# Kernel optimization log

Measured on AMD Instinct MI355X. Metric: run time of the kernel, lower is better.

## Reference

```python
import jax, jax.numpy as jnp
import numpy as np

BN_EPS = 1e-5

def _bn(h, gamma, beta):
    # training-mode BatchNorm1d over node dim, biased variance (as torch)
    m = jnp.mean(h, axis=0)
    v = jnp.var(h, axis=0)
    return (h - m) * jax.lax.rsqrt(v + BN_EPS) * gamma + beta

def _gin(x, edge_index, W, b, n_nodes):
    # PyG GINConv (eps=0): h = Linear(x + sum_{j in N(i)} x_j)
    src, dst = edge_index[0], edge_index[1]
    agg = jax.ops.segment_sum(x[src], dst, num_segments=n_nodes)
    return (x + agg) @ W + b

def setup_inputs() -> dict:
    key = jax.random.key(0)
    ks = jax.random.split(key, 16)
    N, E, D, H, G = 50000, 800000, 128, 256, 64
    x = jax.random.normal(ks[0], (N, D), dtype=jnp.float32)
    edge_index = jax.random.randint(ks[1], (2, E), 0, N, dtype=jnp.int64)
    batch = jnp.sort(jax.random.randint(ks[2], (N,), 0, G, dtype=jnp.int64))
    s = 0.05
    return {
        "x": x, "edge_index": edge_index, "batch": batch, "num_graphs": G,
        "W1": jax.random.normal(ks[3], (D, H), jnp.float32) * s,
        "b1": jnp.zeros((H,), jnp.float32),
        "W2": jax.random.normal(ks[4], (H, H), jnp.float32) * s,
        "b2": jnp.zeros((H,), jnp.float32),
        "W3": jax.random.normal(ks[5], (H, H), jnp.float32) * s,
        "b3": jnp.zeros((H,), jnp.float32),
        "g1": jnp.ones((H,), jnp.float32), "be1": jnp.zeros((H,), jnp.float32),
        "g2": jnp.ones((H,), jnp.float32), "be2": jnp.zeros((H,), jnp.float32),
        "g3": jnp.ones((H,), jnp.float32), "be3": jnp.zeros((H,), jnp.float32),
        "fcW1": jax.random.normal(ks[6], (H, H), jnp.float32) * s,
        "fcb1": jnp.zeros((H,), jnp.float32),
        "fcW2": jax.random.normal(ks[7], (H, 1), jnp.float32) * s,
        "fcb2": jnp.zeros((1,), jnp.float32),
    }

def reference(x, edge_index, batch, num_graphs, W1, b1, W2, b2, W3, b3,
              g1, be1, g2, be2, g3, be3, fcW1, fcb1, fcW2, fcb2):
    n_nodes = x.shape[0]
    # dropout treated as identity (eval / deterministic)
    x1 = jax.nn.relu(_bn(_gin(x, edge_index, W1, b1, n_nodes), g1, be1))
    x2 = jax.nn.relu(_bn(_gin(x1, edge_index, W2, b2, n_nodes), g2, be2)) + x1
    x3 = jax.nn.relu(_bn(_gin(x2, edge_index, W3, b3, n_nodes), g3, be3)) + x2
    # global mean pool over graphs
    sums = jax.ops.segment_sum(x3, batch, num_segments=num_graphs)
    cnt = jax.ops.segment_sum(jnp.ones((n_nodes,), x3.dtype), batch, num_segments=num_graphs)
    pooled = sums / jnp.maximum(cnt, 1.0)[:, None]
    h = jax.nn.relu(pooled @ fcW1 + fcb1)
    return h @ fcW2 + fcb2
```

## Files before the change

### kernel.cpp

```cpp
#include <hip/hip_runtime.h>
#include <hip/hip_bf16.h>
#include <stdint.h>

#define HDIM 256
#define NGRAPH 64
#define NSH 16

typedef short s16x8 __attribute__((ext_vector_type(8)));
typedef float f32x4 __attribute__((ext_vector_type(4)));
typedef unsigned int u32x4 __attribute__((ext_vector_type(4)));

union U8 { u32x4 v; unsigned short s[8]; };

__device__ __forceinline__ float bf2f(unsigned short u){
    union { unsigned int i; float f; } x; x.i = ((unsigned int)u) << 16; return x.f;
}
__device__ __forceinline__ unsigned short f2bf(float f){
    union { float f; unsigned int i; } x; x.f = f;
    unsigned int r = x.i + 0x7fffu + ((x.i >> 16) & 1u);
    return (unsigned short)(r >> 16);
}
__device__ __forceinline__ float ldf(const void* p, int i, int f32){
    return f32 ? ((const float*)p)[i] : bf2f(((const unsigned short*)p)[i]);
}

__global__ void zero_detect_kernel(int* __restrict__ p, int n,
                                   const unsigned short* __restrict__ x,
                                   const int* __restrict__ ei, const int* __restrict__ batch,
                                   int E, int N, int* __restrict__ flags){
    int i = blockIdx.x * 256 + threadIdx.x;
    if (i < n) p[i] = 0;
    if (i == 0){
        int c = 0;
        for (int k = 0; k < 128; k++){
            unsigned e = (x[2 * k] >> 7) & 0xFFu;
            if (e >= 100u && e <= 140u) c++;
        }
        flags[0] = (c < 96) ? 1 : 0;
        int z = (ei[2*E - 1] == 0) && (ei[2*E - 3] == 0) && (ei[2*E - 5] == 0) && (ei[2*E - 7] == 0);
        flags[1] = z ? 1 : 0;
        flags[2] = (batch[N - 1] == 0) ? 1 : 0;
    }
}

__global__ void hist_kernel(const int* __restrict__ ei, int E, int N,
                            const int* __restrict__ flags, int* __restrict__ deg){
    int is64 = flags[1];
    int base = blockIdx.x * 1024;
    #pragma unroll
    for (int k = 0; k < 4; k++){
        int e = base + k * 256 + threadIdx.x;
        if (e < E){
            int d = is64 ? ei[2 * E + 2 * e] : ei[E + e];
            if ((unsigned)d < (unsigned)N) atomicAdd(&deg[d], 1);
        }
    }
}

__global__ void scan1_kernel(const int* __restrict__ deg, int N,
                             int* __restrict__ incl, int* __restrict__ bsums){
    __shared__ int sm[256];
    int t = threadIdx.x;
    int i = blockIdx.x * 256 + t;
    int v = (i < N) ? deg[i] : 0;
    sm[t] = v; __syncthreads();
    for (int off = 1; off < 256; off <<= 1){
        int tv = (t >= off) ? sm[t - off] : 0;
        __syncthreads();
        sm[t] += tv;
        __syncthreads();
    }
    if (i < N) incl[i] = sm[t];
    if (t == 255) bsums[blockIdx.x] = sm[255];
}

__global__ void scan23_kernel(const int* __restrict__ deg, int N, int E, int nb,
                              const int* __restrict__ bsums, int* __restrict__ rowptr){
    __shared__ int sm[256];
    int t = threadIdx.x;
    int bid = blockIdx.x;
    sm[t] = (t < nb && t < bid) ? bsums[t] : 0;
    __syncthreads();
    for (int s = 128; s > 0; s >>= 1){
        if (t < s) sm[t] += sm[t + s];
        __syncthreads();
    }
    int prefix = sm[0];
    int i = bid * 256 + t;
    if (i < N) rowptr[i] = rowptr[i] - deg[i] + prefix;
    if (i == 0) rowptr[N] = E;
}

__global__ void fill_kernel(const int* __restrict__ ei, int E, int N,
                            const int* __restrict__ flags,
                            const int* __restrict__ rowptr, int* __restrict__ fillc,
                            int* __restrict__ csr){
    int is64 = flags[1];
    int base = blockIdx.x * 1024;
    #pragma unroll
    for (int k = 0; k < 4; k++){
        int e = base + k * 256 + threadIdx.x;
        if (e < E){
            int d = is64 ? ei[2 * E + 2 * e] : ei[E + e];
            int s = is64 ? ei[2 * e]         : ei[e];
            if ((unsigned)d < (unsigned)N){
                int p = atomicAdd(&fillc[d], 1);
                csr[rowptr[d] + p] = s;
            }
        }
    }
}

__global__ void prep_kernel(const void* __restrict__ W1, unsigned short* __restrict__ Wp1,
                            const void* __restrict__ W2, unsigned short* __restrict__ Wp2,
                            const void* __restrict__ W3, unsigned short* __restrict__ Wp3,
                            const void* __restrict__ x, unsigned short* __restrict__ Xc,
                            int nx8, const int* __restrict__ flags){
    int bid = blockIdx.x;
    int f32 = flags[0];
    if (bid < 640){
        const void* W; unsigned short* Wp; int base;
        if (bid < 128)      { W = W1; Wp = Wp1; base = bid; }
        else if (bid < 384) { W = W2; Wp = Wp2; base = bid - 128; }
        else                { W = W3; Wp = Wp3; base = bid - 384; }
        int idx = base * 256 + threadIdx.x;
        int k2 = idx & 31;
        int nn = (idx >> 5) & 255;
        int kc = idx >> 13;
        Wp[idx] = f2bf(ldf(W, (kc * 32 + k2) * 256 + nn, f32));
    } else {
        int i = (bid - 640) * 256 + threadIdx.x;
        if (i >= nx8) return;
        int base = i * 8;
        unsigned short o[8];
        if (f32){
            const float* s = (const float*)x + base;
            float4 a = *(const float4*)s;
            float4 b = *(const float4*)(s + 4);
            o[0]=f2bf(a.x); o[1]=f2bf(a.y); o[2]=f2bf(a.z); o[3]=f2bf(a.w);
            o[4]=f2bf(b.x); o[5]=f2bf(b.y); o[6]=f2bf(b.z); o[7]=f2bf(b.w);
        } else {
            *(uint4*)o = *(const uint4*)((const unsigned short*)x + base);
        }
        *(uint4*)&Xc[base] = *(uint4*)o;
    }
}

template<int C>
__global__ __launch_bounds__(256) void agg_vec(const unsigned short* __restrict__ feat, int ldi,
                                               const int* __restrict__ rowptr, const int* __restrict__ csr,
                                               unsigned short* __restrict__ Y, int ldo,
                                               int n0, int n1){
    constexpr int L   = C / 8;
    constexpr int NPB = 256 / L;
    int node = n0 + blockIdx.x * NPB + threadIdx.x / L;
    int lane = threadIdx.x & (L - 1);
    if (node >= n1) return;
    int c0 = lane * 8;
    const unsigned short* base = feat + c0;

    U8 t0; t0.v = *(const u32x4*)&feat[(size_t)node * ldi + c0];
    float acc[8];
    #pragma unroll
    for (int j = 0; j < 8; j++) acc[j] = bf2f(t0.s[j]);

    int lo = rowptr[node], hi = rowptr[node + 1];
    int e = lo;
    for (; e + 3 < hi; e += 4){
        int s0 = csr[e], s1 = csr[e + 1], s2 = csr[e + 2], s3 = csr[e + 3];
        U8 ta, tb, tc, td;
        ta.v = *(const u32x4*)&base[(size_t)s0 * ldi];
        tb.v = *(const u32x4*)&base[(size_t)s1 * ldi];
        tc.v = *(const u32x4*)&base[(size_t)s2 * ldi];
        td.v = *(const u32x4*)&base[(size_t)s3 * ldi];
        #pragma unroll
        for (int j = 0; j < 8; j++)
            acc[j] += (bf2f(ta.s[j]) + bf2f(tb.s[j])) + (bf2f(tc.s[j]) + bf2f(td.s[j]));
    }
    for (; e < hi; e++){
        int s0 = csr[e];
        U8 ta; ta.v = *(const u32x4*)&base[(size_t)s0 * ldi];
        #pragma unroll
        for (int j = 0; j < 8; j++) acc[j] += bf2f(ta.s[j]);
    }
    U8 o;
    #pragma unroll
    for (int j = 0; j < 8; j++) o.s[j] = f2bf(acc[j]);
    *(u32x4*)&Y[(size_t)node * ldo + c0] = o.v;
}

#define CSTR 264
__global__ __launch_bounds__(256) void gemm_tile(
    unsigned short* __restrict__ AC, int K,
    const unsigned short* __restrict__ Bp, const void* __restrict__ bias,
    int M, const int* __restrict__ flags,
    float* __restrict__ S, float* __restrict__ Q)
{
    __shared__ __align__(16) unsigned short smem[64 * CSTR];
    __shared__ float sS[256], sQ[256];
    unsigned short* As = smem;
    unsigned short* Bs = smem + 2560;
    const int tid  = threadIdx.x;
    const int wave = tid >> 6, lane = tid & 63;
    const int quad = lane >> 4, l16 = lane & 15;
    const int m0   = blockIdx.x * 64;
    const int wn   = wave * 64;
    const bool full = (m0 + 64 <= M);
    const int f32  = flags[0];

    const f32x4 zero4 = {0.f, 0.f, 0.f, 0.f};
    f32x4 acc[4][4];
    #pragma unroll
    for (int i = 0; i < 4; i++)
        #pragma unroll
        for (int j = 0; j < 4; j++) acc[i][j] = zero4;

    const int nchunk = K >> 5;
    for (int kc8 = 0; kc8 < nchunk; kc8++){
        int kc = kc8 * 32;
        {
            int r = tid >> 2, cc = (tid & 3) * 8;
            int gr = m0 + r;
            uint4 va; va.x = va.y = va.z = va.w = 0u;
            if (full || gr < M) va = *(const uint4*)&AC[(size_t)gr * HDIM + kc + cc];
            *(uint4*)&As[r * 40 + cc] = va;
        }
        {
            const unsigned short* bc = Bp + (size_t)kc8 * 8192;
            #pragma unroll
            for (int j = 0; j < 4; j++){
                int c = tid + j * 256;
                int n = c >> 2, seg = (c & 3) * 8;
                *(uint4*)&Bs[n * 40 + seg] = *(const uint4*)&bc[c * 8];
            }
        }
        __syncthreads();
        s16x8 af[4], bfr[4];
        #pragma unroll
        for (int mt = 0; mt < 4; mt++)
            af[mt] = *(const s16x8*)&As[(mt * 16 + l16) * 40 + quad * 8];
        #pragma unroll
        for (int nt = 0; nt < 4; nt++)
            bfr[nt] = *(const s16x8*)&Bs[(wn + nt * 16 + l16) * 40 + quad * 8];
        #pragma unroll
        for (int mt = 0; mt < 4; mt++)
            #pragma unroll
            for (int nt = 0; nt < 4; nt++)
                acc[mt][nt] = __builtin_amdgcn_mfma_f32_16x16x32_bf16(af[mt], bfr[nt], acc[mt][nt], 0, 0, 0);
        __syncthreads();
    }
    #pragma unroll
    for (int nt = 0; nt < 4; nt++){
        int gc = wn + nt * 16 + l16;
        float bv = ldf(bias, gc, f32);
        float ps = 0.f, pq = 0.f;
        #pragma unroll
        for (int mt = 0; mt < 4; mt++){
            #pragma unroll
            for (int r = 0; r < 4; r++){
                int lr = mt * 16 + quad * 4 + r;
                float val = acc[mt][nt][r] + bv;
                smem[lr * CSTR + gc] = f2bf(val);
                if (full || (m0 + lr) < M){ ps += val; pq += val * val; }
            }
        }
        ps += __shfl_xor(ps, 16); ps += __shfl_xor(ps, 32);
        pq += __shfl_xor(pq, 16); pq += __shfl_xor(pq, 32);
        if (quad == 0){ sS[gc] = ps; sQ[gc] = pq; }
    }
    __syncthreads();
    #pragma unroll
    for (int j = 0; j < 8; j++){
        int lin = j * 256 + tid;
        int row = lin >> 5, coll = (lin & 31) * 8;
        int gr = m0 + row;
        if (full || gr < M)
            *(uint4*)&AC[(size_t)gr * HDIM + coll] = *(const uint4*)&smem[row * CSTR + coll];
    }
    int sid = (blockIdx.x & (NSH - 1)) * 256 + tid;
    atomicAdd(&S[sid], sS[tid]);
    atomicAdd(&Q[sid], sQ[tid]);
}

__global__ void bnrelu_kernel(const unsigned short* __restrict__ Hin,
                              const float* __restrict__ S, const float* __restrict__ Q,
                              const void* __restrict__ g, const void* __restrict__ be,
                              float invM, const int* __restrict__ flags,
                              const unsigned short* __restrict__ res,
                              unsigned short* __restrict__ Out, int total16){
    __shared__ float sscale[256], sshift[256];
    int tid = threadIdx.x;
    {
        int f32 = flags[0];
        float s = 0.f, q = 0.f;
        #pragma unroll
        for (int k = 0; k < NSH; k++){ s += S[k * 256 + tid]; q += Q[k * 256 + tid]; }
        float m  = s * invM;
        float v  = q * invM - m * m;
        float sc = ldf(g, tid, f32) * rsqrtf(v + 1e-5f);
        sscale[tid] = sc;
        sshift[tid] = ldf(be, tid, f32) - m * sc;
    }
    __syncthreads();
    int idx = blockIdx.x * 256 + tid;
    if (idx >= total16) return;
    #pragma unroll
    for (int h = 0; h < 2; h++){
        int base = idx * 16 + h * 8;
        int c = base & (HDIM - 1);
        unsigned short hv[8], rv[8], ov[8];
        *(uint4*)hv = *(const uint4*)&Hin[base];
        if (res) *(uint4*)rv = *(const uint4*)&res[base];
        #pragma unroll
        for (int j = 0; j < 8; j++){
            float v = bf2f(hv[j]) * sscale[c + j] + sshift[c + j];
            v = (v < 0.f) ? 0.f : v;
            if (res) v += bf2f(rv[j]);
            ov[j] = f2bf(v);
        }
        *(uint4*)&Out[base] = *(uint4*)ov;
    }
}

__global__ __launch_bounds__(256) void bnrelu_pool_kernel(
    const unsigned short* __restrict__ H, const unsigned short* __restrict__ res,
    const float* __restrict__ S, const float* __restrict__ Q,
    const void* __restrict__ g, const void* __restrict__ be,
    float invM, const int* __restrict__ flags,
    const int* __restrict__ batch, int N, float* __restrict__ sums)
{
    __shared__ float lsc[256], lsh[256];
    __shared__ float red[8 * 256];
    int tid = threadIdx.x;
    {
        int f32 = flags[0];
        float s = 0.f, q = 0.f;
        #pragma unroll
        for (int k = 0; k < NSH; k++){ s += S[k * 256 + tid]; q += Q[k * 256 + tid]; }
        float m  = s * invM;
        float v  = q * invM - m * m;
        float sc = ldf(g, tid, f32) * rsqrtf(v + 1e-5f);
        lsc[tid] = sc;
        lsh[tid] = ldf(be, tid, f32) - m * sc;
    }
    __syncthreads();
    int r0 = blockIdx.x * 64;
    if (r0 >= N) return;
    int r1 = min(r0 + 64, N);
    int stride = flags[2] ? 2 : 1;
    int gfirst = batch[r0 * stride];
    int glast  = batch[(r1 - 1) * stride];
    int w  = tid >> 5;
    int c0 = (tid & 31) * 8;
    float sc[8], sh[8];
    #pragma unroll
    for (int j = 0; j < 8; j++){ sc[j] = lsc[c0 + j]; sh[j] = lsh[c0 + j]; }

    float acc[8];
    #pragma unroll
    for (int j = 0; j < 8; j++) acc[j] = 0.f;

    if (gfirst == glast){
        for (int r = r0 + w; r < r1; r += 8){
            U8 hv, rv;
            hv.v = *(const u32x4*)&H[(size_t)r * HDIM + c0];
            rv.v = *(const u32x4*)&res[(size_t)r * HDIM + c0];
            #pragma unroll
            for (int j = 0; j < 8; j++){
                float v = bf2f(hv.s[j]) * sc[j] + sh[j];
                v = (v < 0.f) ? 0.f : v;
                acc[j] += v + bf2f(rv.s[j]);
            }
        }
        *(float4*)&red[w * 256 + c0]     = make_float4(acc[0], acc[1], acc[2], acc[3]);
        *(float4*)&red[w * 256 + c0 + 4] = make_float4(acc[4], acc[5], acc[6], acc[7]);
        __syncthreads();
        float tot = 0.f;
        #pragma unroll
        for (int k = 0; k < 8; k++) tot += red[k * 256 + tid];
        atomicAdd(&sums[gfirst * HDIM + tid], tot);
    } else {
        int curg = batch[min(r0 + w, r1 - 1) * stride];
        for (int r = r0 + w; r < r1; r += 8){
            int gg = batch[r * stride];
            if (gg != curg){
                #pragma unroll
                for (int j = 0; j < 8; j++){
                    if (acc[j] != 0.f) atomicAdd(&sums[curg * HDIM + c0 + j], acc[j]);
                    acc[j] = 0.f;
                }
                curg = gg;
            }
            U8 hv, rv;
            hv.v = *(const u32x4*)&H[(size_t)r * HDIM + c0];
            rv.v = *(const u32x4*)&res[(size_t)r * HDIM + c0];
            #pragma unroll
            for (int j = 0; j < 8; j++){
                float v = bf2f(hv.s[j]) * sc[j] + sh[j];
                v = (v < 0.f) ? 0.f : v;
                acc[j] += v + bf2f(rv.s[j]);
            }
        }
        #pragma unroll
        for (int j = 0; j < 8; j++)
            if (acc[j] != 0.f) atomicAdd(&sums[curg * HDIM + c0 + j], acc[j]);
    }
}

__global__ __launch_bounds__(256) void head_kernel(const float* __restrict__ sums,
                                                   const int* __restrict__ batch, int N,
                                                   const void* __restrict__ fcW1,
                                                   const void* __restrict__ fcb1,
                                                   const void* __restrict__ fcW2,
                                                   const void* __restrict__ fcb2,
                                                   void* __restrict__ out,
                                                   const int* __restrict__ flags){
    __shared__ float sp[256];
    __shared__ float red[256];
    __shared__ int scnt;
    int g = blockIdx.x, j = threadIdx.x;
    int f32 = flags[0];
    int stride = flags[2] ? 2 : 1;
    if (j == 0){
        int lo = 0, hi = N;
        while (lo < hi){ int mid = (lo + hi) >> 1; if (batch[mid * stride] < g) lo = mid + 1; else hi = mid; }
        int a = lo;
        lo = 0; hi = N;
        while (lo < hi){ int mid = (lo + hi) >> 1; if (batch[mid * stride] < g + 1) lo = mid + 1; else hi = mid; }
        scnt = lo - a;
    }
    __syncthreads();
    sp[j] = sums[g * HDIM + j] / (float)max(scnt, 1);
    __syncthreads();
    float acc = ldf(fcb1, j, f32);
    for (int k = 0; k < HDIM; k++) acc += sp[k] * ldf(fcW1, k * HDIM + j, f32);
    acc = (acc < 0.f) ? 0.f : acc;
    red[j] = acc * ldf(fcW2, j, f32);
    __syncthreads();
    for (int s = 128; s > 0; s >>= 1){
        if (j < s) red[j] += red[j + s];
        __syncthreads();
    }
    if (j == 0){
        float r = red[0] + ldf(fcb2, 0, f32);
        if (f32) ((float*)out)[g] = r;
        else     ((unsigned short*)out)[g] = f2bf(r);
    }
}

extern "C" void kernel_launch(void* const* d_in, const int* in_sizes, int n_in,
                              void* d_out, int out_size, void* d_ws, size_t ws_size,
                              hipStream_t stream)
{
    const unsigned short* x    = (const unsigned short*)d_in[0];
    const int*            ei   = (const int*)d_in[1];
    const int*            batch= (const int*)d_in[2];
    const void* W1   = d_in[4];
    const void* b1   = d_in[5];
    const void* W2   = d_in[6];
    const void* b2   = d_in[7];
    const void* W3   = d_in[8];
    const void* b3   = d_in[9];
    const void* g1   = d_in[10];
    const void* be1  = d_in[11];
    const void* g2   = d_in[12];
    const void* be2  = d_in[13];
    const void* g3   = d_in[14];
    const void* be3  = d_in[15];
    const void* fcW1 = d_in[16];
    const void* fcb1 = d_in[17];
    const void* fcW2 = d_in[18];
    const void* fcb2 = d_in[19];

    const int N = in_sizes[0] / 128;
    const int E = in_sizes[1] / 2;
    const int D = 128;

    char* p = (char*)d_ws;
    int*   deg     = (int*)p;   p += (size_t)N * 4;
    int*   fillc   = (int*)p;   p += (size_t)N * 4;
    float* stats   = (float*)p; p += 6 * NSH * 256 * 4;
    float* poolsum = (float*)p; p += NGRAPH * HDIM * 4;
    size_t zbytes  = (size_t)(p - (char*)d_ws);
    int*   flags   = (int*)p;   p += 16 * 4;
    int*   bsums   = (int*)p;   p += 256 * 4;
    int*   rowptr  = (int*)p;   p += ((size_t)N + 4) * 4;
    int*   csr     = (int*)p;   p += (size_t)E * 4;
    unsigned short* Wp1 = (unsigned short*)p; p += 256 * 128 * 2;
    unsigned short* Wp2 = (unsigned short*)p; p += 256 * 256 * 2;
    unsigned short* Wp3 = (unsigned short*)p; p += 256 * 256 * 2;
    unsigned short* B1  = (unsigned short*)p; p += (size_t)N * HDIM * 2;
    unsigned short* B2  = (unsigned short*)p; p += (size_t)N * HDIM * 2;
    unsigned short* Xc  = B1;

    float* S0 = stats + 0 * NSH * 256; float* Q0 = stats + 1 * NSH * 256;
    float* S1 = stats + 2 * NSH * 256; float* Q1 = stats + 3 * NSH * 256;
    float* S2 = stats + 4 * NSH * 256; float* Q2 = stats + 5 * NSH * 256;

    const int nbN = (N + 255) / 256;
    const int nbE4 = (E + 1023) / 1024;
    const int gM64  = (N + 63) / 64;
    const float invM = 1.0f / (float)N;
    const int total16 = N * HDIM / 16;
    const int zn = (int)(zbytes / 4);
    const int nx8 = N * D / 8;
    const int half = N / 2;

    zero_detect_kernel<<<(zn + 255) / 256, 256, 0, stream>>>((int*)d_ws, zn, x, ei, batch, E, N, flags);

    hist_kernel<<<nbE4, 256, 0, stream>>>(ei, E, N, flags, deg);
    scan1_kernel<<<nbN, 256, 0, stream>>>(deg, N, rowptr, bsums);
    scan23_kernel<<<nbN, 256, 0, stream>>>(deg, N, E, nbN, bsums, rowptr);
    fill_kernel<<<nbE4, 256, 0, stream>>>(ei, E, N, flags, rowptr, fillc, csr);

    prep_kernel<<<640 + (nx8 + 255) / 256, 256, 0, stream>>>(W1, Wp1, W2, Wp2, W3, Wp3, x, Xc, nx8, flags);

    agg_vec<128><<<(half + 15) / 16, 256, 0, stream>>>(Xc, D, rowptr, csr, B2, HDIM, 0, half);
    agg_vec<128><<<(N - half + 15) / 16, 256, 0, stream>>>(Xc, D, rowptr, csr, B2, HDIM, half, N);
    gemm_tile<<<gM64, 256, 0, stream>>>(B2, 128, Wp1, b1, N, flags, S0, Q0);
    bnrelu_kernel<<<(total16 + 255) / 256, 256, 0, stream>>>(
        B2, S0, Q0, g1, be1, invM, flags, (const unsigned short*)nullptr, B1, total16);

    agg_vec<256><<<(half + 7) / 8, 256, 0, stream>>>(B1, HDIM, rowptr, csr, B2, HDIM, 0, half);
    agg_vec<256><<<(N - half + 7) / 8, 256, 0, stream>>>(B1, HDIM, rowptr, csr, B2, HDIM, half, N);
    gemm_tile<<<gM64, 256, 0, stream>>>(B2, 256, Wp2, b2, N, flags, S1, Q1);
    bnrelu_kernel<<<(total16 + 255) / 256, 256, 0, stream>>>(
        B2, S1, Q1, g2, be2, invM, flags, B1, B1, total16);

    agg_vec<256><<<(half + 7) / 8, 256, 0, stream>>>(B1, HDIM, rowptr, csr, B2, HDIM, 0, half);
    agg_vec<256><<<(N - half + 7) / 8, 256, 0, stream>>>(B1, HDIM, rowptr, csr, B2, HDIM, half, N);
    gemm_tile<<<gM64, 256, 0, stream>>>(B2, 256, Wp3, b3, N, flags, S2, Q2);
    bnrelu_pool_kernel<<<gM64, 256, 0, stream>>>(
        B2, B1, S2, Q2, g3, be3, invM, flags, batch, N, poolsum);

    head_kernel<<<NGRAPH, 256, 0, stream>>>(poolsum, batch, N, fcW1, fcb1, fcW2, fcb2, d_out, flags);

    (void)n_in; (void)out_size; (void)ws_size;
}
```

Baseline: 526.2 us.

## Enlarge GEMM tile to 128 rows with 2x2 wave layout; merge split aggregation launches

The GEMM block now computes a 128x256 tile using a 2x2 wave grid, each wave covering 64x128. This doubles B-operand reuse per block and halves the number of blocks. The epilogue is written back in two 64-row passes through shared memory, with per-column stats accumulated by shared atomics. The aggregation kernel is also launched once over all nodes instead of as two half-range launches. Risks are higher register pressure from the 32 accumulators and lower occupancy, plus fewer blocks (~391) across the CUs.

```diff
diff --git a/kernel.cpp b/kernel.cpp
--- a/kernel.cpp
+++ b/kernel.cpp
@@ -5,6 +5,7 @@
 #define HDIM 256
 #define NGRAPH 64
 #define NSH 16
+#define CSTR 264
 
 typedef short s16x8 __attribute__((ext_vector_type(8)));
 typedef float f32x4 __attribute__((ext_vector_type(4)));
@@ -149,13 +150,12 @@
 template<int C>
 __global__ __launch_bounds__(256) void agg_vec(const unsigned short* __restrict__ feat, int ldi,
                                                const int* __restrict__ rowptr, const int* __restrict__ csr,
-                                               unsigned short* __restrict__ Y, int ldo,
-                                               int n0, int n1){
+                                               unsigned short* __restrict__ Y, int ldo, int N){
     constexpr int L   = C / 8;
     constexpr int NPB = 256 / L;
-    int node = n0 + blockIdx.x * NPB + threadIdx.x / L;
+    int node = blockIdx.x * NPB + threadIdx.x / L;
     int lane = threadIdx.x & (L - 1);
-    if (node >= n1) return;
+    if (node >= N) return;
     int c0 = lane * 8;
     const unsigned short* base = feat + c0;
 
@@ -189,7 +189,6 @@
     *(u32x4*)&Y[(size_t)node * ldo + c0] = o.v;
 }
 
-#define CSTR 264
 __global__ __launch_bounds__(256) void gemm_tile(
     unsigned short* __restrict__ AC, int K,
     const unsigned short* __restrict__ Bp, const void* __restrict__ bias,
@@ -199,27 +198,32 @@
     __shared__ __align__(16) unsigned short smem[64 * CSTR];
     __shared__ float sS[256], sQ[256];
     unsigned short* As = smem;
-    unsigned short* Bs = smem + 2560;
+    unsigned short* Bs = smem + 5120;
     const int tid  = threadIdx.x;
     const int wave = tid >> 6, lane = tid & 63;
     const int quad = lane >> 4, l16 = lane & 15;
-    const int m0   = blockIdx.x * 64;
-    const int wn   = wave * 64;
-    const bool full = (m0 + 64 <= M);
+    const int m0   = blockIdx.x * 128;
+    const int wm   = (wave & 1) * 64;
+    const int wn   = (wave >> 1) * 128;
+    const bool full = (m0 + 128 <= M);
     const int f32  = flags[0];
 
+    sS[tid] = 0.f; sQ[tid] = 0.f;
+
     const f32x4 zero4 = {0.f, 0.f, 0.f, 0.f};
-    f32x4 acc[4][4];
+    f32x4 acc[4][8];
     #pragma unroll
     for (int i = 0; i < 4; i++)
         #pragma unroll
-        for (int j = 0; j < 4; j++) acc[i][j] = zero4;
+        for (int j = 0; j < 8; j++) acc[i][j] = zero4;
 
     const int nchunk = K >> 5;
     for (int kc8 = 0; kc8 < nchunk; kc8++){
         int kc = kc8 * 32;
-        {
-            int r = tid >> 2, cc = (tid & 3) * 8;
+        #pragma unroll
+        for (int j = 0; j < 2; j++){
+            int c = tid + j * 256;
+            int r = c >> 2, cc = (c & 3) * 8;
             int gr = m0 + r;
             uint4 va; va.x = va.y = va.z = va.w = 0u;
             if (full || gr < M) va = *(const uint4*)&AC[(size_t)gr * HDIM + kc + cc];
@@ -235,47 +239,53 @@
             }
         }
         __syncthreads();
-        s16x8 af[4], bfr[4];
+        s16x8 af[4];
         #pragma unroll
         for (int mt = 0; mt < 4; mt++)
-            af[mt] = *(const s16x8*)&As[(mt * 16 + l16) * 40 + quad * 8];
-        #pragma unroll
-        for (int nt = 0; nt < 4; nt++)
-            bfr[nt] = *(const s16x8*)&Bs[(wn + nt * 16 + l16) * 40 + quad * 8];
-        #pragma unroll
-        for (int mt = 0; mt < 4; mt++)
+            af[mt] = *(const s16x8*)&As[(wm + mt * 16 + l16) * 40 + quad * 8];
+        #pragma unroll
+        for (int nt = 0; nt < 8; nt++){
+            s16x8 b = *(const s16x8*)&Bs[(wn + nt * 16 + l16) * 40 + quad * 8];
             #pragma unroll
-            for (int nt = 0; nt < 4; nt++)
-                acc[mt][nt] = __builtin_amdgcn_mfma_f32_16x16x32_bf16(af[mt], bfr[nt], acc[mt][nt], 0, 0, 0);
-        __syncthreads();
-    }
-    #pragma unroll
-    for (int nt = 0; nt < 4; nt++){
-        int gc = wn + nt * 16 + l16;
-        float bv = ldf(bias, gc, f32);
-        float ps = 0.f, pq = 0.f;
-        #pragma unroll
-        for (int mt = 0; mt < 4; mt++){
+            for (int mt = 0; mt < 4; mt++)
+                acc[mt][nt] = __builtin_amdgcn_mfma_f32_16x16x32_bf16(af[mt], b, acc[mt][nt], 0, 0, 0);
+        }
+        __syncthreads();
+    }
+    #pragma unroll
+    for (int pass = 0; pass < 2; pass++){
+        if ((wave & 1) == pass){
             #pragma unroll
-            for (int r = 0; r < 4; r++){
-                int lr = mt * 16 + quad * 4 + r;
-                float val = acc[mt][nt][r] + bv;
-                smem[lr * CSTR + gc] = f2bf(val);
-                if (full || (m0 + lr) < M){ ps += val; pq += val * val; }
+            for (int nt = 0; nt < 8; nt++){
+                int gc = wn + nt * 16 + l16;
+                float bv = ldf(bias, gc, f32);
+                float ps = 0.f, pq = 0.f;
+                #pragma unroll
+                for (int mt = 0; mt < 4; mt++){
+                    #pragma unroll
+                    for (int r = 0; r < 4; r++){
+                        int lr = mt * 16 + quad * 4 + r;
+                        int gr = m0 + pass * 64 + lr;
+                        float val = acc[mt][nt][r] + bv;
+                        smem[lr * CSTR + gc] = f2bf(val);
+                        if (full || gr < M){ ps += val; pq += val * val; }
+                    }
+                }
+                ps += __shfl_xor(ps, 16); ps += __shfl_xor(ps, 32);
+                pq += __shfl_xor(pq, 16); pq += __shfl_xor(pq, 32);
+                if (quad == 0){ atomicAdd(&sS[gc], ps); atomicAdd(&sQ[gc], pq); }
             }
         }
-        ps += __shfl_xor(ps, 16); ps += __shfl_xor(ps, 32);
-        pq += __shfl_xor(pq, 16); pq += __shfl_xor(pq, 32);
-        if (quad == 0){ sS[gc] = ps; sQ[gc] = pq; }
-    }
-    __syncthreads();
-    #pragma unroll
-    for (int j = 0; j < 8; j++){
-        int lin = j * 256 + tid;
-        int row = lin >> 5, coll = (lin & 31) * 8;
-        int gr = m0 + row;
-        if (full || gr < M)
-            *(uint4*)&AC[(size_t)gr * HDIM + coll] = *(const uint4*)&smem[row * CSTR + coll];
+        __syncthreads();
+        #pragma unroll
+        for (int j = 0; j < 8; j++){
+            int lin = j * 256 + tid;
+            int row = lin >> 5, coll = (lin & 31) * 8;
+            int gr = m0 + pass * 64 + row;
+            if (full || gr < M)
+                *(uint4*)&AC[(size_t)gr * HDIM + coll] = *(const uint4*)&smem[row * CSTR + coll];
+        }
+        __syncthreads();
     }
     int sid = (blockIdx.x & (NSH - 1)) * 256 + tid;
     atomicAdd(&S[sid], sS[tid]);
@@ -499,12 +509,12 @@
 
     const int nbN = (N + 255) / 256;
     const int nbE4 = (E + 1023) / 1024;
+    const int gM128 = (N + 127) / 128;
     const int gM64  = (N + 63) / 64;
     const float invM = 1.0f / (float)N;
     const int total16 = N * HDIM / 16;
     const int zn = (int)(zbytes / 4);
     const int nx8 = N * D / 8;
-    const int half = N / 2;
 
     zero_detect_kernel<<<(zn + 255) / 256, 256, 0, stream>>>((int*)d_ws, zn, x, ei, batch, E, N, flags);
 
@@ -515,21 +525,18 @@
 
     prep_kernel<<<640 + (nx8 + 255) / 256, 256, 0, stream>>>(W1, Wp1, W2, Wp2, W3, Wp3, x, Xc, nx8, flags);
 
-    agg_vec<128><<<(half + 15) / 16, 256, 0, stream>>>(Xc, D, rowptr, csr, B2, HDIM, 0, half);
-    agg_vec<128><<<(N - half + 15) / 16, 256, 0, stream>>>(Xc, D, rowptr, csr, B2, HDIM, half, N);
-    gemm_tile<<<gM64, 256, 0, stream>>>(B2, 128, Wp1, b1, N, flags, S0, Q0);
+    agg_vec<128><<<(N + 15) / 16, 256, 0, stream>>>(Xc, D, rowptr, csr, B2, HDIM, N);
+    gemm_tile<<<gM128, 256, 0, stream>>>(B2, 128, Wp1, b1, N, flags, S0, Q0);
     bnrelu_kernel<<<(total16 + 255) / 256, 256, 0, stream>>>(
         B2, S0, Q0, g1, be1, invM, flags, (const unsigned short*)nullptr, B1, total16);
 
-    agg_vec<256><<<(half + 7) / 8, 256, 0, stream>>>(B1, HDIM, rowptr, csr, B2, HDIM, 0, half);
-    agg_vec<256><<<(N - half + 7) / 8, 256, 0, stream>>>(B1, HDIM, rowptr, csr, B2, HDIM, half, N);
-    gemm_tile<<<gM64, 256, 0, stream>>>(B2, 256, Wp2, b2, N, flags, S1, Q1);
+    agg_vec<256><<<(N + 7) / 8, 256, 0, stream>>>(B1, HDIM, rowptr, csr, B2, HDIM, N);
+    gemm_tile<<<gM128, 256, 0, stream>>>(B2, 256, Wp2, b2, N, flags, S1, Q1);
     bnrelu_kernel<<<(total16 + 255) / 256, 256, 0, stream>>>(
         B2, S1, Q1, g2, be2, invM, flags, B1, B1, total16);
 
-    agg_vec<256><<<(half + 7) / 8, 256, 0, stream>>>(B1, HDIM, rowptr, csr, B2, HDIM, 0, half);
-    agg_vec<256><<<(N - half + 7) / 8, 256, 0, stream>>>(B1, HDIM, rowptr, csr, B2, HDIM, half, N);
-    gemm_tile<<<gM64, 256, 0, stream>>>(B2, 256, Wp3, b3, N, flags, S2, Q2);
+    agg_vec<256><<<(N + 7) / 8, 256, 0, stream>>>(B1, HDIM, rowptr, csr, B2, HDIM, N);
+    gemm_tile<<<gM128, 256, 0, stream>>>(B2, 256, Wp3, b3, N, flags, S2, Q2);
     bnrelu_pool_kernel<<<gM64, 256, 0, stream>>>(
         B2, B1, S2, Q2, g3, be3, invM, flags, batch, N, poolsum);
 
```

After: 566.7 us. +7.7%, slower.
